# Kernel optimization log

Hardware: AMD Instinct MI355X
Metric: run time of the kernel (lower is better)

Reference implementation:

```python
import jax, jax.numpy as jnp
import numpy as np

B, L, D = 32, 64, 768  # batch, len_arg, in_dim == h_dim (bert-base)


def setup_inputs() -> dict:
    key = jax.random.key(0)
    k = jax.random.split(key, 7)
    out_a1 = jax.random.normal(k[0], (B, L, D), jnp.float32)
    out_a2 = jax.random.normal(k[1], (B, L, D), jnp.float32)
    # content lengths l in [8, L-2]; mask sum = l + 2 (CLS/SEP), so mask fits in L
    len1 = jax.random.randint(k[2], (B,), 8, L - 1)
    len2 = jax.random.randint(k[3], (B,), 8, L - 1)
    pos = jnp.arange(L)[None, :]
    mask_arg1 = (pos < (len1 + 2)[:, None]).astype(jnp.int32)
    mask_arg2 = (pos < (len2 + 2)[:, None]).astype(jnp.int32)
    s = 1.0 / np.sqrt(D)
    we_w = jax.random.normal(k[4], (1, D), jnp.float32) * s
    fc_w = jax.random.normal(k[5], (2 * D, D), jnp.float32) * s
    fc_b = jnp.zeros((2 * D,), jnp.float32)
    return {"out_a1": out_a1, "out_a2": out_a2, "mask_arg1": mask_arg1,
            "mask_arg2": mask_arg2, "we_w": we_w, "fc_w": fc_w, "fc_b": fc_b}


def _build_matrix(out_a1, out_a2, mask_arg1, mask_arg2):
    # Vectorized form of the per-batch python loop: for flat index
    # kk = i*l2 + j (i < l1, j < l2), matrix[b, kk] = a1[b, 1+i] - a2[b, 1+j];
    # rest padded with zeros.
    l1 = jnp.sum(mask_arg1, axis=1) - 2  # (B,)
    l2 = jnp.sum(mask_arg2, axis=1) - 2  # (B,)
    kk = jnp.arange(L * L)[None, :]      # (1, L*L)
    i = kk // l2[:, None]                # (B, L*L)
    j = kk % l2[:, None]
    valid = kk < (l1 * l2)[:, None]
    i_c = jnp.clip(i + 1, 0, L - 1)
    j_c = jnp.clip(j + 1, 0, L - 1)
    w1 = jnp.take_along_axis(out_a1, i_c[:, :, None], axis=1)  # (B, L*L, D)
    w2 = jnp.take_along_axis(out_a2, j_c[:, :, None], axis=1)
    return jnp.where(valid[:, :, None], w1 - w2, 0.0)


def reference(out_a1, out_a2, mask_arg1, mask_arg2, we_w, fc_w, fc_b):
    matrix = _build_matrix(out_a1, out_a2, mask_arg1, mask_arg2)  # (B, L*L, D)
    We_ = jnp.einsum('bkd,d->bk', matrix, we_w[0])                # (B, L*L)
    masked = jnp.where(jnp.abs(We_) < 1e-7, -1e7, We_)
    alpha = jax.nn.softmax(masked, axis=1)
    pooled = jnp.einsum('bk,bkd->bd', alpha, matrix)              # (B, D)
    out = jnp.tanh(pooled @ fc_w.T + fc_b)                        # (B, 2D)
    return out  # dropout is identity in eval mode
```

## Files before the change

### kernel.cpp

```cpp
#include <hip/hip_runtime.h>
#include <math.h>

#define L_  64
#define D_  768
#define B_  32
#define OD_ 1536
#define NW  8
#define NT  512

__device__ __forceinline__ float wsum(float v) {
#pragma unroll
    for (int off = 32; off > 0; off >>= 1) v += __shfl_xor(v, off, 64);
    return v;
}
__device__ __forceinline__ float wmaxr(float v) {
#pragma unroll
    for (int off = 32; off > 0; off >>= 1) v = fmaxf(v, __shfl_xor(v, off, 64));
    return v;
}
__device__ __forceinline__ int wsumi(int v) {
#pragma unroll
    for (int off = 32; off > 0; off >>= 1) v += __shfl_xor(v, off, 64);
    return v;
}

__global__ __launch_bounds__(NT) void pooled_kernel(
    const float* __restrict__ a1, const float* __restrict__ a2,
    const int* __restrict__ m1, const int* __restrict__ m2,
    const float* __restrict__ we, float* __restrict__ pooled)
{
    const int b    = blockIdx.x;
    const int t    = threadIdx.x;
    const int lane = t & 63;
    const int wave = t >> 6;

    __shared__ float s1[L_], s2[L_];
    __shared__ float rowsum[L_], colsum[L_];
    __shared__ float colpart[NW][L_];
    __shared__ float wm[NW];
    __shared__ float sZ;
    __shared__ int   sl1, sl2;

    if (wave == 0) {
        int s = wsumi(m1[b * L_ + lane]);
        if (lane == 0) sl1 = s - 2;
    } else if (wave == 1) {
        int s = wsumi(m2[b * L_ + lane]);
        if (lane == 0) sl2 = s - 2;
    }
    if (t < L_) rowsum[t] = 0.f;

    float wv[12];
#pragma unroll
    for (int k = 0; k < 12; k++) wv[k] = we[lane + 64 * k];

    __syncthreads();
    const int l1 = sl1, l2 = sl2;

    for (int r = wave; r < 2 * L_; r += NW) {
        const int which = r >> 6;
        const int i     = r & 63;
        const int len   = which ? l2 : l1;
        float val = 0.f;
        if (i < len) {
            const float* row = (which ? a2 : a1) + ((size_t)b * L_ + 1 + i) * D_;
            float acc = 0.f;
#pragma unroll
            for (int k = 0; k < 12; k++) acc = fmaf(row[lane + 64 * k], wv[k], acc);
            val = wsum(acc);
        }
        if (lane == 0) { if (which) s2[i] = val; else s1[i] = val; }
    }
    __syncthreads();

    const float s2v = s2[lane];
    const bool  jok = (lane < l2);

    float lm = -1e30f;
    for (int i = wave; i < l1; i += NW) {
        float v = s1[i] - s2v;
        if (jok && fabsf(v) >= 1e-7f) lm = fmaxf(lm, v);
    }
    lm = wmaxr(lm);
    if (lane == 0) wm[wave] = lm;
    __syncthreads();
    float m = wm[0];
#pragma unroll
    for (int w = 1; w < NW; w++) m = fmaxf(m, wm[w]);

    float colacc = 0.f;
    for (int i = wave; i < l1; i += NW) {
        float v = s1[i] - s2v;
        float e = (jok && fabsf(v) >= 1e-7f) ? __expf(v - m) : 0.f;
        float rs = wsum(e);
        if (lane == 0) rowsum[i] = rs;
        colacc += e;
    }
    colpart[wave][lane] = colacc;
    __syncthreads();

    if (wave == 0) {
        float c = 0.f;
#pragma unroll
        for (int w = 0; w < NW; w++) c += colpart[w][lane];
        colsum[lane] = c;
        float Z = wsum(c);
        if (lane == 0) sZ = Z;
    }
    __syncthreads();
    const float invZ = 1.0f / sZ;

    for (int d = t; d < D_; d += NT) {
        float acc = 0.f;
        const float* p1 = a1 + ((size_t)b * L_ + 1) * D_ + d;
        for (int i = 0; i < l1; i++) acc = fmaf(rowsum[i], p1[(size_t)i * D_], acc);
        const float* p2 = a2 + ((size_t)b * L_ + 1) * D_ + d;
        for (int j = 0; j < l2; j++) acc = fmaf(-colsum[j], p2[(size_t)j * D_], acc);
        pooled[b * D_ + d] = acc * invZ;
    }
}

__global__ __launch_bounds__(256) void fc_kernel(
    const float* __restrict__ pooled, const float* __restrict__ fc_w,
    const float* __restrict__ fc_b, float* __restrict__ out)
{
    const int t = threadIdx.x;
    const int b = t & 31;
    const int o = blockIdx.x * 8 + (t >> 5);

    const float4* wr = (const float4*)(fc_w + (size_t)o * D_);
    const float4* pr = (const float4*)(pooled + (size_t)b * D_);
    float acc0 = 0.f, acc1 = 0.f;
#pragma unroll 8
    for (int k = 0; k < D_ / 8; k++) {
        float4 w = wr[2 * k],     p = pr[2 * k];
        acc0 = fmaf(w.x, p.x, fmaf(w.y, p.y, fmaf(w.z, p.z, fmaf(w.w, p.w, acc0))));
        float4 w2 = wr[2 * k + 1], p2 = pr[2 * k + 1];
        acc1 = fmaf(w2.x, p2.x, fmaf(w2.y, p2.y, fmaf(w2.z, p2.z, fmaf(w2.w, p2.w, acc1))));
    }
    out[b * OD_ + o] = tanhf(acc0 + acc1 + fc_b[o]);
}

extern "C" void kernel_launch(void* const* d_in, const int* in_sizes, int n_in,
                              void* d_out, int out_size, void* d_ws, size_t ws_size,
                              hipStream_t stream) {
    const float* a1  = (const float*)d_in[0];
    const float* a2  = (const float*)d_in[1];
    const int*   m1  = (const int*)d_in[2];
    const int*   m2  = (const int*)d_in[3];
    const float* we  = (const float*)d_in[4];
    const float* fcw = (const float*)d_in[5];
    const float* fcb = (const float*)d_in[6];
    float*       out = (float*)d_out;

    float* pooled = (float*)d_ws;

    pooled_kernel<<<B_, NT, 0, stream>>>(a1, a2, m1, m2, we, pooled);
    fc_kernel<<<OD_ / 8, 256, 0, stream>>>(pooled, fcw, fcb, out);
}
```

Measured before the change: 123.4 us.

## Split pooled kernel into parallel score kernel and D-chunked pooling kernel

The single per-batch kernel (32 blocks) is split into a score kernel with one wave per row across 1024 blocks, writing scores to workspace, and a pooling kernel that splits D into three chunks per batch (96 blocks). The aim is to spread work over far more CUs, since 32 blocks leave most of the GPU idle. The costs are an extra launch, a workspace round trip for scores, and softmax statistics recomputed in each of the three chunks.

```diff
diff --git a/kernel.cpp b/kernel.cpp
--- a/kernel.cpp
+++ b/kernel.cpp
@@ -5,8 +5,6 @@
 #define D_  768
 #define B_  32
 #define OD_ 1536
-#define NW  8
-#define NT  512
 
 __device__ __forceinline__ float wsum(float v) {
 #pragma unroll
@@ -24,20 +22,44 @@
     return v;
 }
 
-__global__ __launch_bounds__(NT) void pooled_kernel(
+__global__ __launch_bounds__(256) void score_kernel(
+    const float* __restrict__ a1, const float* __restrict__ a2,
+    const float* __restrict__ we, float* __restrict__ s1ws,
+    float* __restrict__ s2ws)
+{
+    const int lane = threadIdx.x & 63;
+    const int wave = threadIdx.x >> 6;
+    const int b    = blockIdx.x >> 5;
+    const int slot = ((blockIdx.x & 31) << 2) + wave;
+    const int which = slot >> 6;
+    const int i     = slot & 63;
+    if (i >= 63) return;
+
+    const float* row = (which ? a2 : a1) + ((size_t)b * L_ + 1 + i) * D_ + lane;
+    const float* w   = we + lane;
+    float acc = 0.f;
+#pragma unroll
+    for (int k = 0; k < 12; k++) acc = fmaf(row[64 * k], w[64 * k], acc);
+    acc = wsum(acc);
+    if (lane == 0) (which ? s2ws : s1ws)[b * L_ + i] = acc;
+}
+
+#define NW2 4
+__global__ __launch_bounds__(256) void pool_kernel(
     const float* __restrict__ a1, const float* __restrict__ a2,
     const int* __restrict__ m1, const int* __restrict__ m2,
-    const float* __restrict__ we, float* __restrict__ pooled)
+    const float* __restrict__ s1ws, const float* __restrict__ s2ws,
+    float* __restrict__ pooled)
 {
-    const int b    = blockIdx.x;
-    const int t    = threadIdx.x;
-    const int lane = t & 63;
-    const int wave = t >> 6;
+    const int b     = blockIdx.x / 3;
+    const int chunk = blockIdx.x % 3;
+    const int t     = threadIdx.x;
+    const int lane  = t & 63;
+    const int wave  = t >> 6;
 
-    __shared__ float s1[L_], s2[L_];
     __shared__ float rowsum[L_], colsum[L_];
-    __shared__ float colpart[NW][L_];
-    __shared__ float wm[NW];
+    __shared__ float colpart[NW2][L_];
+    __shared__ float wm[NW2];
     __shared__ float sZ;
     __shared__ int   sl1, sl2;
 
@@ -48,37 +70,15 @@
         int s = wsumi(m2[b * L_ + lane]);
         if (lane == 0) sl2 = s - 2;
     }
-    if (t < L_) rowsum[t] = 0.f;
-
-    float wv[12];
-#pragma unroll
-    for (int k = 0; k < 12; k++) wv[k] = we[lane + 64 * k];
-
     __syncthreads();
     const int l1 = sl1, l2 = sl2;
 
-    for (int r = wave; r < 2 * L_; r += NW) {
-        const int which = r >> 6;
-        const int i     = r & 63;
-        const int len   = which ? l2 : l1;
-        float val = 0.f;
-        if (i < len) {
-            const float* row = (which ? a2 : a1) + ((size_t)b * L_ + 1 + i) * D_;
-            float acc = 0.f;
-#pragma unroll
-            for (int k = 0; k < 12; k++) acc = fmaf(row[lane + 64 * k], wv[k], acc);
-            val = wsum(acc);
-        }
-        if (lane == 0) { if (which) s2[i] = val; else s1[i] = val; }
-    }
-    __syncthreads();
-
-    const float s2v = s2[lane];
+    const float s2v = s2ws[b * L_ + lane];
     const bool  jok = (lane < l2);
 
     float lm = -1e30f;
-    for (int i = wave; i < l1; i += NW) {
-        float v = s1[i] - s2v;
+    for (int i = wave; i < l1; i += NW2) {
+        float v = s1ws[b * L_ + i] - s2v;
         if (jok && fabsf(v) >= 1e-7f) lm = fmaxf(lm, v);
     }
     lm = wmaxr(lm);
@@ -86,11 +86,11 @@
     __syncthreads();
     float m = wm[0];
 #pragma unroll
-    for (int w = 1; w < NW; w++) m = fmaxf(m, wm[w]);
+    for (int w = 1; w < NW2; w++) m = fmaxf(m, wm[w]);
 
     float colacc = 0.f;
-    for (int i = wave; i < l1; i += NW) {
-        float v = s1[i] - s2v;
+    for (int i = wave; i < l1; i += NW2) {
+        float v = s1ws[b * L_ + i] - s2v;
         float e = (jok && fabsf(v) >= 1e-7f) ? __expf(v - m) : 0.f;
         float rs = wsum(e);
         if (lane == 0) rowsum[i] = rs;
@@ -98,11 +98,10 @@
     }
     colpart[wave][lane] = colacc;
     __syncthreads();
-
     if (wave == 0) {
         float c = 0.f;
 #pragma unroll
-        for (int w = 0; w < NW; w++) c += colpart[w][lane];
+        for (int w = 0; w < NW2; w++) c += colpart[w][lane];
         colsum[lane] = c;
         float Z = wsum(c);
         if (lane == 0) sZ = Z;
@@ -110,14 +109,13 @@
     __syncthreads();
     const float invZ = 1.0f / sZ;
 
-    for (int d = t; d < D_; d += NT) {
-        float acc = 0.f;
-        const float* p1 = a1 + ((size_t)b * L_ + 1) * D_ + d;
-        for (int i = 0; i < l1; i++) acc = fmaf(rowsum[i], p1[(size_t)i * D_], acc);
-        const float* p2 = a2 + ((size_t)b * L_ + 1) * D_ + d;
-        for (int j = 0; j < l2; j++) acc = fmaf(-colsum[j], p2[(size_t)j * D_], acc);
-        pooled[b * D_ + d] = acc * invZ;
-    }
+    const int d = chunk * 256 + t;
+    const float* p1 = a1 + ((size_t)b * L_ + 1) * D_ + d;
+    const float* p2 = a2 + ((size_t)b * L_ + 1) * D_ + d;
+    float acc = 0.f;
+    for (int i = 0; i < l1; i++) acc = fmaf(rowsum[i], p1[(size_t)i * D_], acc);
+    for (int j = 0; j < l2; j++) acc = fmaf(-colsum[j], p2[(size_t)j * D_], acc);
+    pooled[b * D_ + d] = acc * invZ;
 }
 
 __global__ __launch_bounds__(256) void fc_kernel(
@@ -133,7 +131,7 @@
     float acc0 = 0.f, acc1 = 0.f;
 #pragma unroll 8
     for (int k = 0; k < D_ / 8; k++) {
-        float4 w = wr[2 * k],     p = pr[2 * k];
+        float4 w = wr[2 * k],      p = pr[2 * k];
         acc0 = fmaf(w.x, p.x, fmaf(w.y, p.y, fmaf(w.z, p.z, fmaf(w.w, p.w, acc0))));
         float4 w2 = wr[2 * k + 1], p2 = pr[2 * k + 1];
         acc1 = fmaf(w2.x, p2.x, fmaf(w2.y, p2.y, fmaf(w2.z, p2.z, fmaf(w2.w, p2.w, acc1))));
@@ -153,8 +151,11 @@
     const float* fcb = (const float*)d_in[6];
     float*       out = (float*)d_out;
 
-    float* pooled = (float*)d_ws;
+    float* s1ws   = (float*)d_ws;
+    float* s2ws   = s1ws + B_ * L_;
+    float* pooled = s2ws + B_ * L_;
 
-    pooled_kernel<<<B_, NT, 0, stream>>>(a1, a2, m1, m2, we, pooled);
+    score_kernel<<<B_ * 32, 256, 0, stream>>>(a1, a2, we, s1ws, s2ws);
+    pool_kernel<<<B_ * 3, 256, 0, stream>>>(a1, a2, m1, m2, s1ws, s2ws, pooled);
     fc_kernel<<<OD_ / 8, 256, 0, stream>>>(pooled, fcw, fcb, out);
 }
```

Result: no change. 122.5 us (-0.7%).
